# Performance work log

Hardware: AMD Instinct MI355X
Metric: run time of the kernel (lower is better)

The kernel has to match this reference:

```python
import jax, jax.numpy as jnp
import numpy as np

MU = 255          # mu-law levels - 1
H = 64            # block_hidden_size
SKIP = 256        # skip_size
NL = 24           # num_layers
CYC = 6           # cycle_size -> dilation = 2**(i % CYC)
UPK = 4           # upsample conv kernel/stride
REP = 75          # upsample repeat
LF = 80           # local_features_size
B = 2
LLEN = 64                      # local (spectrogram) frames
SLEN = LLEN * UPK * REP        # 19200 signal samples


def setup_inputs() -> dict:
    key = jax.random.key(0)
    ks = jax.random.split(key, 16)
    s = 0.1
    rn = lambda k, shape: jax.random.normal(k, shape, jnp.float32) * s
    return {
        "local_features": jax.random.normal(ks[0], (B, LLEN, LF), jnp.float32),
        "gold_signal": jax.random.randint(ks[1], (B, SLEN), 0, MU + 1, jnp.int32),
        "embed_W": rn(ks[2], (H, MU + 1)),          # 1x1 conv (mu+1 -> H), as matrix
        "embed_b": rn(ks[3], (H,)),
        "up_W": rn(ks[4], (LF, LF, UPK)),           # ConvTranspose1d weight [in, out, k]
        "up_b": rn(ks[5], (LF,)),
        "cond_W": rn(ks[6], (NL * 2 * H, LF)),      # 1x1 conv LF -> NL*2H
        "cond_b": rn(ks[7], (NL * 2 * H,)),
        "dil_W": rn(ks[8], (NL, 2 * H, H, 2)),      # dilated causal conv, kernel 2
        "dil_b": rn(ks[9], (NL, 2 * H)),
        "skip_W": rn(ks[10], (NL, SKIP, H)),
        "skip_b": rn(ks[11], (NL, SKIP)),
        "res_W": rn(ks[12], (NL - 1, H, H)),        # no residual conv on last layer
        "res_b": rn(ks[13], (NL - 1, H)),
        "out_W1": rn(ks[14], (MU + 1, SKIP)),       # out conv 1 (no bias)
        "out_W2": rn(ks[15], (MU + 1, MU + 1)),     # out conv 2 (no bias)
    }


def reference(local_features, gold_signal, embed_W, embed_b, up_W, up_b,
              cond_W, cond_b, dil_W, dil_b, skip_W, skip_b, res_W, res_b,
              out_W1, out_W2):
    Bv = local_features.shape[0]
    # --- conditional features upsample ---
    x = jnp.transpose(local_features, (0, 2, 1))                     # [B, LF, Lloc]
    # ConvTranspose1d with kernel == stride == UPK: each frame emits UPK frames
    up = jnp.einsum('bct,cok->botk', x, up_W).reshape(Bv, LF, -1)    # [B, LF, Lloc*UPK]
    up = up + up_b[None, :, None]
    up = jnp.repeat(up, REP, axis=-1)                                # [B, LF, SLEN]
    cond = jnp.einsum('oc,bct->bot', cond_W, up) + cond_b[None, :, None]
    L = cond.shape[-1]
    cond = cond.reshape(Bv, NL, 2 * H, L)                            # per-layer 2H channels
    # --- embed mu-law one-hot signal (one-hot matmul == gather) ---
    sig = jnp.transpose(embed_W[:, gold_signal], (1, 0, 2)) + embed_b[None, :, None]  # [B, H, L]
    # --- residual blocks ---
    skip_sum = jnp.zeros((Bv, SKIP, L), cond.dtype)
    for i in range(NL):
        d = 2 ** (i % CYC)
        prev = jnp.pad(sig, ((0, 0), (0, 0), (d, 0)))[:, :, :L]      # causal shift by dilation
        a = (jnp.einsum('oc,bct->bot', dil_W[i, :, :, 0], prev)
             + jnp.einsum('oc,bct->bot', dil_W[i, :, :, 1], sig)
             + dil_b[i][None, :, None] + cond[:, i])
        z = jnp.tanh(a[:, :H]) * jax.nn.sigmoid(a[:, H:])            # gated activation
        skip_sum = skip_sum + jnp.einsum('oc,bct->bot', skip_W[i], z) + skip_b[i][None, :, None]
        if i < NL - 1:
            sig = sig + jnp.einsum('oc,bct->bot', res_W[i], z) + res_b[i][None, :, None]
    # --- output head: ReLU -> 1x1 -> ReLU -> 1x1 -> log_softmax over levels ---
    h = jax.nn.relu(skip_sum)
    h = jax.nn.relu(jnp.einsum('oc,bct->bot', out_W1, h))
    logits = jnp.einsum('oc,bct->bot', out_W2, h)
    return jax.nn.log_softmax(logits, axis=1)                        # [B, mu+1, SLEN]
```

## Files before the change

kernel.cpp:

```cpp
#include <hip/hip_runtime.h>
#include <math.h>

#define MU1   256
#define H     64
#define H2    128
#define SKIPC 256
#define NL    24
#define LF    80
#define UPK   4
#define REP   75
#define BB    2
#define LLEN  64
#define LL    19200

using bf16x8 = __attribute__((ext_vector_type(8))) short;
using bf16x4 = __attribute__((ext_vector_type(4))) short;
using f32x4  = __attribute__((ext_vector_type(4))) float;

__device__ __forceinline__ float b2f(short s) {
    union { unsigned u; float f; } v; v.u = ((unsigned)(unsigned short)s) << 16; return v.f;
}
__device__ __forceinline__ short f2b(float f) {
    union { float f; unsigned u; } v; v.f = f;
    unsigned r = (v.u + 0x7fff + ((v.u >> 16) & 1)) >> 16;
    return (short)r;
}

__global__ __launch_bounds__(256) void prep_kernel(
    const float* __restrict__ dil_W,  const float* __restrict__ skip_W,
    const float* __restrict__ res_W,  const float* __restrict__ embed_W,
    const float* __restrict__ embed_b,const float* __restrict__ cond_W,
    const float* __restrict__ out_W1, const float* __restrict__ out_W2,
    const float* __restrict__ skip_b,
    short* __restrict__ dil_Wb, short* __restrict__ skip_Wb,
    short* __restrict__ res_Wb, short* __restrict__ embed_allb,
    float* __restrict__ cond_Wt, short* __restrict__ W1b,
    short* __restrict__ W2b, float* __restrict__ sbsum)
{
    int idx = blockIdx.x * 256 + threadIdx.x;
    const int n1 = NL * 2 * H2 * H;
    const int n2 = NL * SKIPC * H;
    const int n3 = (NL - 1) * H * H;
    const int n4 = MU1 * H;
    const int n5 = LF * NL * H2;
    const int n6 = MU1 * SKIPC;
    const int n7 = MU1 * MU1;
    if (idx < n1) {
        int c = idx & 63; int o = (idx >> 6) & 127;
        int k = (idx >> 13) & 1; int i = idx >> 14;
        dil_Wb[idx] = f2b(dil_W[((i * H2 + o) * H + c) * 2 + k]);
        return;
    }
    idx -= n1;
    if (idx < n2) { skip_Wb[idx] = f2b(skip_W[idx]); return; }
    idx -= n2;
    if (idx < n3) { res_Wb[idx] = f2b(res_W[idx]); return; }
    idx -= n3;
    if (idx < n4) {
        int h = idx & 63; int g = idx >> 6;
        embed_allb[idx] = f2b(embed_W[h * MU1 + g] + embed_b[h]);
        return;
    }
    idx -= n4;
    if (idx < n5) {
        int o = idx % (NL * H2); int c = idx / (NL * H2);
        cond_Wt[idx] = cond_W[o * LF + c];
        return;
    }
    idx -= n5;
    if (idx < n6) { W1b[idx] = f2b(out_W1[idx]); return; }
    idx -= n6;
    if (idx < n7) { W2b[idx] = f2b(out_W2[idx]); return; }
    idx -= n7;
    if (idx < SKIPC) {
        float a = 0.f;
        for (int i = 0; i < NL; i++) a += skip_b[i * SKIPC + idx];
        sbsum[idx] = a;
        return;
    }
}

__global__ __launch_bounds__(256) void embed_kernel(
    const int* __restrict__ gold, const short* __restrict__ eW,
    short* __restrict__ sig)
{
    int idx = blockIdx.x * 256 + threadIdx.x;
    if (idx >= BB * LL * 8) return;
    int ch = idx & 7; int bt = idx >> 3;
    int g = gold[bt];
    *(bf16x8*)(sig + (size_t)bt * H + ch * 8) = *(const bf16x8*)(eW + g * H + ch * 8);
}

__global__ __launch_bounds__(256) void cond_kernel(
    const float* __restrict__ lf, const float* __restrict__ up_W,
    const float* __restrict__ up_b, const float* __restrict__ cond_Wt,
    const float* __restrict__ cond_b, const float* __restrict__ dil_b,
    float* __restrict__ condS)
{
    __shared__ float s_up[LF];
    int j = blockIdx.x;
    int ot = blockIdx.y;
    int b = blockIdx.z;
    int frame = j >> 2, k = j & 3;
    int tid = threadIdx.x;
    if (tid < LF) {
        float a = up_b[tid];
        const float* lfr = lf + (b * LLEN + frame) * LF;
        #pragma unroll 8
        for (int c = 0; c < LF; ++c) a += lfr[c] * up_W[(c * LF + tid) * UPK + k];
        s_up[tid] = a;
    }
    __syncthreads();
    int o = ot * 256 + tid;
    float a = cond_b[o] + dil_b[o];
    #pragma unroll 8
    for (int c = 0; c < LF; ++c) a += cond_Wt[c * 3072 + o] * s_up[c];
    condS[((size_t)(b * 256 + j)) * 3072 + o] = a;
}

template<int DA, int DB, bool LASTPAIR>
__global__ __launch_bounds__(256) void pair_mfma(
    const short* __restrict__ sig_in, short* __restrict__ sig_out,
    short* __restrict__ z_grp,
    const short* __restrict__ dil_Wb_all,
    const short* __restrict__ res_Wb_all,
    const float* __restrict__ res_b_all,
    const float* __restrict__ condS,
    int p)
{
    __shared__ __align__(16) short sa[144][72];
    __shared__ __align__(16) short sb[128][72];
    __shared__ __align__(16) short sz[128][72];
    __shared__ float scond[2][3][128];

    const int iA = 2 * p, iB = 2 * p + 1;
    const int ilA = iA & 7, ilB = iB & 7;
    const int b = blockIdx.y;
    const int t0 = blockIdx.x * 96;
    const int tid = threadIdx.x;
    const int w = tid >> 6;
    const int lane = tid & 63;
    const int lr = lane & 15, lg = lane >> 4;
    const int c0 = (t0 >= 32) ? (t0 - 32) / 75 : 0;

    {
        const short* basein = sig_in + (size_t)b * LL * H;
        #pragma unroll
        for (int it = 0; it < 5; ++it) {
            int task = tid + it * 256;
            if (task < 1152) {
                int r = task >> 3, ch = task & 7;
                int t = t0 - 48 + r;
                bf16x8 v = {};
                if (t >= 0) v = *(const bf16x8*)(basein + (size_t)t * H + ch * 8);
                *(bf16x8*)&sa[r][ch * 8] = v;
            }
        }
        #pragma unroll
        for (int it = 0; it < 3; ++it) {
            int task = tid + it * 256;
            int sel = task >= 384;
            int cj = (task - sel * 384) >> 7;
            int o = task & 127;
            int col = c0 + cj; col = col > 255 ? 255 : col;
            scond[sel][cj][o] = condS[((size_t)(b * 256 + col)) * 3072 + (iA + sel) * 128 + o];
        }
    }
    __syncthreads();

    {
        const short* dW = dil_Wb_all + (size_t)iA * 2 * H2 * H;
        f32x4 acc[2][8];
        #pragma unroll
        for (int m = 0; m < 2; ++m)
            #pragma unroll
            for (int n = 0; n < 8; ++n) acc[m][n] = (f32x4){0.f, 0.f, 0.f, 0.f};
        bf16x8 afA[2][4];
        #pragma unroll
        for (int m = 0; m < 2; ++m) {
            int rc = 16 + 16 * (2 * w + m) + lr;
            afA[m][0] = *(const bf16x8*)&sa[rc - DA][lg * 8];
            afA[m][1] = *(const bf16x8*)&sa[rc - DA][32 + lg * 8];
            afA[m][2] = *(const bf16x8*)&sa[rc][lg * 8];
            afA[m][3] = *(const bf16x8*)&sa[rc][32 + lg * 8];
        }
        #pragma unroll
        for (int n = 0; n < 8; ++n)
            #pragma unroll
            for (int kk = 0; kk < 4; ++kk) {
                bf16x8 bw = *(const bf16x8*)(dW + (((kk >> 1) * H2 + 16 * n + lr) * H) + (kk & 1) * 32 + lg * 8);
                acc[0][n] = __builtin_amdgcn_mfma_f32_16x16x32_bf16(afA[0][kk], bw, acc[0][n], 0, 0, 0);
                acc[1][n] = __builtin_amdgcn_mfma_f32_16x16x32_bf16(afA[1][kk], bw, acc[1][n], 0, 0, 0);
            }
        #pragma unroll
        for (int m = 0; m < 2; ++m)
            #pragma unroll
            for (int n = 0; n < 4; ++n)
                #pragma unroll
                for (int r = 0; r < 4; ++r) {
                    int relt = -32 + 16 * (2 * w + m) + 4 * lg + r;
                    int t = t0 + relt;
                    int o = 16 * n + lr;
                    short zb = 0;
                    if (t >= 0) {
                        int ci = t / 75 - c0;
                        float av = acc[m][n][r] + scond[0][ci][o];
                        float gv = acc[m][n + 4][r] + scond[0][ci][64 + o];
                        float th = 1.f - 2.f / (__expf(2.f * av) + 1.f);
                        float sg = 1.f / (1.f + __expf(-gv));
                        zb = f2b(th * sg);
                    }
                    sz[relt + 32][o] = zb;
                }
    }
    __syncthreads();

    #pragma unroll
    for (int it = 0; it < 3; ++it) {
        int task = tid + it * 256;
        int r = task >> 3, ch = task & 7;
        *(bf16x8*)(z_grp + ((size_t)(b * LL + t0 + r)) * 512 + ilA * 64 + ch * 8)
            = *(const bf16x8*)&sz[32 + r][ch * 8];
    }

    {
        const short* rW = res_Wb_all + (size_t)iA * H * H;
        const float* rb_ = res_b_all + (size_t)iA * H;
        f32x4 rac[2][4];
        #pragma unroll
        for (int m = 0; m < 2; ++m)
            #pragma unroll
            for (int n = 0; n < 4; ++n) rac[m][n] = (f32x4){0.f, 0.f, 0.f, 0.f};
        bf16x8 za[2][2];
        #pragma unroll
        for (int m = 0; m < 2; ++m) {
            int row = 16 * (2 * w + m) + lr;
            za[m][0] = *(const bf16x8*)&sz[row][lg * 8];
            za[m][1] = *(const bf16x8*)&sz[row][32 + lg * 8];
        }
        #pragma unroll
        for (int n = 0; n < 4; ++n)
            #pragma unroll
            for (int kk = 0; kk < 2; ++kk) {
                bf16x8 bw = *(const bf16x8*)(rW + (16 * n + lr) * H + kk * 32 + lg * 8);
                rac[0][n] = __builtin_amdgcn_mfma_f32_16x16x32_bf16(za[0][kk], bw, rac[0][n], 0, 0, 0);
                rac[1][n] = __builtin_amdgcn_mfma_f32_16x16x32_bf16(za[1][kk], bw, rac[1][n], 0, 0, 0);
            }
        #pragma unroll
        for (int n = 0; n < 4; ++n) {
            float rbv = rb_[16 * n + lr];
            #pragma unroll
            for (int m = 0; m < 2; ++m)
                #pragma unroll
                for (int r = 0; r < 4; ++r) {
                    int relt = -32 + 16 * (2 * w + m) + 4 * lg + r;
                    int t = t0 + relt;
                    int c = 16 * n + lr;
                    short vb = 0;
                    if (t >= 0) vb = f2b(b2f(sa[relt + 48][c]) + rac[m][n][r] + rbv);
                    sb[relt + 32][c] = vb;
                }
        }
    }
    __syncthreads();

    {
        const short* dW = dil_Wb_all + (size_t)iB * 2 * H2 * H;
        f32x4 accF[6], accG[6];
        #pragma unroll
        for (int m = 0; m < 6; ++m) { accF[m] = (f32x4){0.f,0.f,0.f,0.f}; accG[m] = (f32x4){0.f,0.f,0.f,0.f}; }
        bf16x8 bwF[4], bwG[4];
        #pragma unroll
        for (int kk = 0; kk < 4; ++kk) {
            int oF = 16 * w + lr;
            bwF[kk] = *(const bf16x8*)(dW + (((kk >> 1) * H2 + oF) * H) + (kk & 1) * 32 + lg * 8);
            bwG[kk] = *(const bf16x8*)(dW + (((kk >> 1) * H2 + 64 + oF) * H) + (kk & 1) * 32 + lg * 8);
        }
        #pragma unroll
        for (int m = 0; m < 6; ++m) {
            int rc = 32 + 16 * m + lr;
            bf16x8 af[4];
            af[0] = *(const bf16x8*)&sb[rc - DB][lg * 8];
            af[1] = *(const bf16x8*)&sb[rc - DB][32 + lg * 8];
            af[2] = *(const bf16x8*)&sb[rc][lg * 8];
            af[3] = *(const bf16x8*)&sb[rc][32 + lg * 8];
            #pragma unroll
            for (int kk = 0; kk < 4; ++kk)
                accF[m] = __builtin_amdgcn_mfma_f32_16x16x32_bf16(af[kk], bwF[kk], accF[m], 0, 0, 0);
            #pragma unroll
            for (int kk = 0; kk < 4; ++kk)
                accG[m] = __builtin_amdgcn_mfma_f32_16x16x32_bf16(af[kk], bwG[kk], accG[m], 0, 0, 0);
        }
        #pragma unroll
        for (int m = 0; m < 6; ++m)
            #pragma unroll
            for (int r = 0; r < 4; ++r) {
                int relt = 16 * m + 4 * lg + r;
                int t = t0 + relt;
                int o = 16 * w + lr;
                int ci = t / 75 - c0;
                float av = accF[m][r] + scond[1][ci][o];
                float gv = accG[m][r] + scond[1][ci][64 + o];
                float th = 1.f - 2.f / (__expf(2.f * av) + 1.f);
                float sg = 1.f / (1.f + __expf(-gv));
                sz[relt][o] = f2b(th * sg);
            }
    }
    __syncthreads();

    #pragma unroll
    for (int it = 0; it < 3; ++it) {
        int task = tid + it * 256;
        int r = task >> 3, ch = task & 7;
        *(bf16x8*)(z_grp + ((size_t)(b * LL + t0 + r)) * 512 + ilB * 64 + ch * 8)
            = *(const bf16x8*)&sz[r][ch * 8];
    }

    if (!LASTPAIR) {
        const short* rW = res_Wb_all + (size_t)iB * H * H;
        const float* rb_ = res_b_all + (size_t)iB * H;
        int c = 16 * w + lr;
        f32x4 rac[6];
        #pragma unroll
        for (int m = 0; m < 6; ++m) rac[m] = (f32x4){0.f, 0.f, 0.f, 0.f};
        bf16x8 bwR[2];
        bwR[0] = *(const bf16x8*)(rW + c * H + lg * 8);
        bwR[1] = *(const bf16x8*)(rW + c * H + 32 + lg * 8);
        #pragma unroll
        for (int m = 0; m < 6; ++m) {
            bf16x8 z0 = *(const bf16x8*)&sz[16 * m + lr][lg * 8];
            bf16x8 z1 = *(const bf16x8*)&sz[16 * m + lr][32 + lg * 8];
            rac[m] = __builtin_amdgcn_mfma_f32_16x16x32_bf16(z0, bwR[0], rac[m], 0, 0, 0);
            rac[m] = __builtin_amdgcn_mfma_f32_16x16x32_bf16(z1, bwR[1], rac[m], 0, 0, 0);
        }
        float rbv = rb_[c];
        #pragma unroll
        for (int m = 0; m < 6; ++m)
            #pragma unroll
            for (int r = 0; r < 4; ++r) {
                int relt = 16 * m + 4 * lg + r;
                sa[relt][c] = f2b(b2f(sb[relt + 32][c]) + rac[m][r] + rbv);
            }
        __syncthreads();
        #pragma unroll
        for (int it = 0; it < 3; ++it) {
            int task = tid + it * 256;
            int r = task >> 3, ch = task & 7;
            *(bf16x8*)(sig_out + ((size_t)(b * LL + t0 + r)) * H + ch * 8)
                = *(const bf16x8*)&sa[r][ch * 8];
        }
    }
}

template<bool G0>
__global__ __launch_bounds__(256) void skip_gemm(
    const short* __restrict__ z_grp, const short* __restrict__ sWb,
    float* __restrict__ skipS)
{
    __shared__ __align__(16) short s_a[64][136];
    const int b = blockIdx.y;
    const int t0 = blockIdx.x * 64;
    const int tid = threadIdx.x;
    const int w = tid >> 6;
    const int lane = tid & 63;
    const int lr = lane & 15, lg = lane >> 4;

    f32x4 acc[4][4];
    #pragma unroll
    for (int mt = 0; mt < 4; ++mt)
        #pragma unroll
        for (int nt = 0; nt < 4; ++nt) acc[mt][nt] = (f32x4){0.f, 0.f, 0.f, 0.f};

    for (int chunk = 0; chunk < 4; ++chunk) {
        __syncthreads();
        #pragma unroll
        for (int it = 0; it < 4; ++it) {
            int task = tid + it * 256;
            int r = task >> 4, ch = task & 15;
            *(bf16x8*)&s_a[r][ch * 8] =
                *(const bf16x8*)(z_grp + ((size_t)(b * LL + t0 + r)) * 512 + chunk * 128 + ch * 8);
        }
        __syncthreads();
        bf16x8 bw[4][4];
        #pragma unroll
        for (int nt = 0; nt < 4; ++nt)
            #pragma unroll
            for (int kk = 0; kk < 4; ++kk) {
                int layer = 2 * chunk + (kk >> 1);
                bw[nt][kk] = *(const bf16x8*)(sWb +
                    ((size_t)(layer * SKIPC + 64 * w + 16 * nt + lr)) * H + (kk & 1) * 32 + 8 * lg);
            }
        #pragma unroll
        for (int mt = 0; mt < 4; ++mt) {
            bf16x8 afr[4];
            #pragma unroll
            for (int kk = 0; kk < 4; ++kk)
                afr[kk] = *(const bf16x8*)&s_a[16 * mt + lr][32 * kk + 8 * lg];
            #pragma unroll
            for (int nt = 0; nt < 4; ++nt)
                #pragma unroll
                for (int kk = 0; kk < 4; ++kk)
                    acc[mt][nt] = __builtin_amdgcn_mfma_f32_16x16x32_bf16(afr[kk], bw[nt][kk], acc[mt][nt], 0, 0, 0);
        }
    }
    #pragma unroll
    for (int mt = 0; mt < 4; ++mt)
        #pragma unroll
        for (int nt = 0; nt < 4; ++nt) {
            int s = 64 * w + 16 * nt + lr;
            #pragma unroll
            for (int reg = 0; reg < 4; ++reg) {
                int t = t0 + 16 * mt + 4 * lg + reg;
                float* p = skipS + ((size_t)(b * LL + t)) * SKIPC + s;
                float v = acc[mt][nt][reg];
                if (!G0) v += *p;
                *p = v;
            }
        }
}

__global__ __launch_bounds__(256) void head_mfma(
    const float* __restrict__ skipS, const float* __restrict__ sbsum,
    const short* __restrict__ W1b, const short* __restrict__ W2b,
    float* __restrict__ out)
{
    __shared__ __align__(16) unsigned char smem[128 * 68 * 4];
    short (*s_x)[264] = (short(*)[264])smem;
    float (*s_o)[68]  = (float(*)[68])smem;
    __shared__ float s_red[4][64];
    __shared__ float s_sb[256];

    const int b = blockIdx.y;
    const int t0 = blockIdx.x * 64;
    const int tid = threadIdx.x;
    const int w = tid >> 6;
    const int lane = tid & 63;
    const int lr = lane & 15, lg = lane >> 4;

    s_sb[tid] = sbsum[tid];
    __syncthreads();

    #pragma unroll
    for (int it = 0; it < 16; ++it) {
        int task = tid + it * 256;
        int r = task >> 6, c4 = task & 63;
        f32x4 v = *(const f32x4*)(skipS + ((size_t)(b * LL + t0 + r)) * SKIPC + c4 * 4);
        bf16x4 o;
        #pragma unroll
        for (int j = 0; j < 4; ++j) o[j] = f2b(fmaxf(v[j] + s_sb[c4 * 4 + j], 0.f));
        *(bf16x4*)&s_x[r][c4 * 4] = o;
    }
    __syncthreads();

    f32x4 acc1[4][4];
    #pragma unroll
    for (int mt = 0; mt < 4; ++mt)
        #pragma unroll
        for (int nt = 0; nt < 4; ++nt) acc1[mt][nt] = (f32x4){0.f, 0.f, 0.f, 0.f};
    #pragma unroll
    for (int kk = 0; kk < 8; ++kk) {
        bf16x8 afr[4];
        #pragma unroll
        for (int mt = 0; mt < 4; ++mt)
            afr[mt] = *(const bf16x8*)&s_x[16 * mt + lr][32 * kk + 8 * lg];
        #pragma unroll
        for (int nt = 0; nt < 4; ++nt) {
            bf16x8 bw = *(const bf16x8*)(W1b + ((size_t)(64 * w + 16 * nt + lr)) * MU1 + 32 * kk + 8 * lg);
            #pragma unroll
            for (int mt = 0; mt < 4; ++mt)
                acc1[mt][nt] = __builtin_amdgcn_mfma_f32_16x16x32_bf16(afr[mt], bw, acc1[mt][nt], 0, 0, 0);
        }
    }
    __syncthreads();
    #pragma unroll
    for (int mt = 0; mt < 4; ++mt)
        #pragma unroll
        for (int nt = 0; nt < 4; ++nt)
            #pragma unroll
            for (int reg = 0; reg < 4; ++reg) {
                int tl = 16 * mt + 4 * lg + reg;
                int o = 64 * w + 16 * nt + lr;
                s_x[tl][o] = f2b(fmaxf(acc1[mt][nt][reg], 0.f));
            }
    __syncthreads();

    f32x4 acc2[4][4];
    #pragma unroll
    for (int mt = 0; mt < 4; ++mt)
        #pragma unroll
        for (int nt = 0; nt < 4; ++nt) acc2[mt][nt] = (f32x4){0.f, 0.f, 0.f, 0.f};
    #pragma unroll
    for (int kk = 0; kk < 8; ++kk) {
        bf16x8 afr[4];
        #pragma unroll
        for (int mt = 0; mt < 4; ++mt)
            afr[mt] = *(const bf16x8*)&s_x[16 * mt + lr][32 * kk + 8 * lg];
        #pragma unroll
        for (int nt = 0; nt < 4; ++nt) {
            bf16x8 bw = *(const bf16x8*)(W2b + ((size_t)(64 * w + 16 * nt + lr)) * MU1 + 32 * kk + 8 * lg);
            #pragma unroll
            for (int mt = 0; mt < 4; ++mt)
                acc2[mt][nt] = __builtin_amdgcn_mfma_f32_16x16x32_bf16(afr[mt], bw, acc2[mt][nt], 0, 0, 0);
        }
    }

    float mv[4][4];
    #pragma unroll
    for (int mt = 0; mt < 4; ++mt)
        #pragma unroll
        for (int reg = 0; reg < 4; ++reg) {
            float m = -3.4e38f;
            #pragma unroll
            for (int nt = 0; nt < 4; ++nt) m = fmaxf(m, acc2[mt][nt][reg]);
            #pragma unroll
            for (int off = 1; off <= 8; off <<= 1) m = fmaxf(m, __shfl_xor(m, off));
            int tl = 16 * mt + 4 * lg + reg;
            if (lr == 0) s_red[w][tl] = m;
        }
    __syncthreads();
    #pragma unroll
    for (int mt = 0; mt < 4; ++mt)
        #pragma unroll
        for (int reg = 0; reg < 4; ++reg) {
            int tl = 16 * mt + 4 * lg + reg;
            mv[mt][reg] = fmaxf(fmaxf(s_red[0][tl], s_red[1][tl]), fmaxf(s_red[2][tl], s_red[3][tl]));
        }
    __syncthreads();
    #pragma unroll
    for (int mt = 0; mt < 4; ++mt)
        #pragma unroll
        for (int reg = 0; reg < 4; ++reg) {
            float s = 0.f;
            #pragma unroll
            for (int nt = 0; nt < 4; ++nt) s += __expf(acc2[mt][nt][reg] - mv[mt][reg]);
            #pragma unroll
            for (int off = 1; off <= 8; off <<= 1) s += __shfl_xor(s, off);
            int tl = 16 * mt + 4 * lg + reg;
            if (lr == 0) s_red[w][tl] = s;
        }
    __syncthreads();
    #pragma unroll
    for (int mt = 0; mt < 4; ++mt)
        #pragma unroll
        for (int reg = 0; reg < 4; ++reg) {
            int tl = 16 * mt + 4 * lg + reg;
            float denom = s_red[0][tl] + s_red[1][tl] + s_red[2][tl] + s_red[3][tl];
            mv[mt][reg] = mv[mt][reg] + __logf(denom);
        }
    __syncthreads();

    #pragma unroll
    for (int pass = 0; pass < 2; ++pass) {
        if ((w >> 1) == pass) {
            #pragma unroll
            for (int mt = 0; mt < 4; ++mt)
                #pragma unroll
                for (int nt = 0; nt < 4; ++nt)
                    #pragma unroll
                    for (int reg = 0; reg < 4; ++reg) {
                        int ch = 64 * (w & 1) + 16 * nt + lr;
                        int tl = 16 * mt + 4 * lg + reg;
                        s_o[ch][tl] = acc2[mt][nt][reg] - mv[mt][reg];
                    }
        }
        __syncthreads();
        {
            int row = tid >> 1, half = tid & 1;
            float* op = out + ((size_t)(b * MU1 + pass * 128 + row)) * LL + t0 + half * 32;
            #pragma unroll
            for (int k = 0; k < 8; ++k)
                *(f32x4*)(op + 4 * k) = *(const f32x4*)&s_o[row][half * 32 + 4 * k];
        }
        __syncthreads();
    }
}

extern "C" void kernel_launch(void* const* d_in, const int* in_sizes, int n_in,
                              void* d_out, int out_size, void* d_ws, size_t ws_size,
                              hipStream_t stream)
{
    const float* lf      = (const float*)d_in[0];
    const int*   gold    = (const int*)  d_in[1];
    const float* embed_W = (const float*)d_in[2];
    const float* embed_b = (const float*)d_in[3];
    const float* up_W    = (const float*)d_in[4];
    const float* up_b    = (const float*)d_in[5];
    const float* cond_W  = (const float*)d_in[6];
    const float* cond_b  = (const float*)d_in[7];
    const float* dil_W   = (const float*)d_in[8];
    const float* dil_b   = (const float*)d_in[9];
    const float* skip_W  = (const float*)d_in[10];
    const float* skip_b  = (const float*)d_in[11];
    const float* res_W   = (const float*)d_in[12];
    const float* res_b   = (const float*)d_in[13];
    const float* W1      = (const float*)d_in[14];
    const float* W2      = (const float*)d_in[15];
    float* out = (float*)d_out;

    unsigned char* p = (unsigned char*)d_ws;
    short* sigA      = (short*)p; p += (size_t)BB * LL * H * 2;
    short* sigB      = (short*)p; p += (size_t)BB * LL * H * 2;
    short* z_grp     = (short*)p; p += (size_t)BB * LL * 512 * 2;
    float* skipS     = (float*)p; p += (size_t)BB * LL * SKIPC * 4;
    float* condS     = (float*)p; p += (size_t)BB * 256 * NL * H2 * 4;
    short* dil_Wb    = (short*)p; p += (size_t)NL * 2 * H2 * H * 2;
    short* skip_Wb   = (short*)p; p += (size_t)NL * SKIPC * H * 2;
    short* res_Wb    = (short*)p; p += (size_t)(NL - 1) * H * H * 2;
    short* embed_allb= (short*)p; p += (size_t)MU1 * H * 2;
    float* cond_Wt   = (float*)p; p += (size_t)LF * NL * H2 * 4;
    short* W1b       = (short*)p; p += (size_t)MU1 * SKIPC * 2;
    short* W2b       = (short*)p; p += (size_t)MU1 * MU1 * 2;
    float* sbsum     = (float*)p; p += (size_t)SKIPC * 4;

    const int prep_n = NL*2*H2*H + NL*SKIPC*H + (NL-1)*H*H + MU1*H + LF*NL*H2 + MU1*SKIPC + MU1*MU1 + SKIPC;
    prep_kernel<<<(prep_n + 255) / 256, 256, 0, stream>>>(
        dil_W, skip_W, res_W, embed_W, embed_b, cond_W, W1, W2, skip_b,
        dil_Wb, skip_Wb, res_Wb, embed_allb, cond_Wt, W1b, W2b, sbsum);

    embed_kernel<<<(BB * LL * 8 + 255) / 256, 256, 0, stream>>>(gold, embed_allb, sigA);

    cond_kernel<<<dim3(256, 12, BB), 256, 0, stream>>>(lf, up_W, up_b, cond_Wt, cond_b, dil_b, condS);

    short* si = sigA;
    short* so = sigB;
    dim3 pgrid(LL / 96, BB);
    dim3 sgrid(LL / 64, BB);
    for (int pp = 0; pp < 12; ++pp) {
        int r3 = pp % 3;
        if (r3 == 0)
            pair_mfma<1, 2, false><<<pgrid, 256, 0, stream>>>(si, so, z_grp, dil_Wb, res_Wb, res_b, condS, pp);
        else if (r3 == 1)
            pair_mfma<4, 8, false><<<pgrid, 256, 0, stream>>>(si, so, z_grp, dil_Wb, res_Wb, res_b, condS, pp);
        else if (pp == 11)
            pair_mfma<16, 32, true><<<pgrid, 256, 0, stream>>>(si, so, z_grp, dil_Wb, res_Wb, res_b, condS, pp);
        else
            pair_mfma<16, 32, false><<<pgrid, 256, 0, stream>>>(si, so, z_grp, dil_Wb, res_Wb, res_b, condS, pp);
        short* tmp = si; si = so; so = tmp;

        if ((pp & 3) == 3) {
            int g = pp >> 2;
            const short* sWb = skip_Wb + (size_t)g * 8 * SKIPC * H;
            if (g == 0)
                skip_gemm<true><<<sgrid, 256, 0, stream>>>(z_grp, sWb, skipS);
            else
                skip_gemm<false><<<sgrid, 256, 0, stream>>>(z_grp, sWb, skipS);
        }
    }

    head_mfma<<<sgrid, 256, 0, stream>>>(skipS, sbsum, W1b, W2b, out);
}
```

Before: 591.1 us.

## Merge skip GEMM into following pair kernel via extra blocks and double-buffered z

Double-buffers the z group buffer so the skip GEMM for one group of 8 layers can run as extra blocks inside the next pair_mfma launch instead of as a separate launch. This removes two kernel launches and their serialisation, letting skip accumulation overlap with the residual-block work. It also halves the head kernel's time tile to 32 to launch more blocks. It needs extra workspace and falls back to the old schedule when the workspace is too small.

```diff
diff --git a/kernel.cpp b/kernel.cpp
--- a/kernel.cpp
+++ b/kernel.cpp
@@ -118,10 +118,84 @@
     condS[((size_t)(b * 256 + j)) * 3072 + o] = a;
 }
 
-template<int DA, int DB, bool LASTPAIR>
+template<bool G0>
+__device__ __forceinline__ void skip_body(
+    const short* __restrict__ z_grp, const short* __restrict__ sWb,
+    float* __restrict__ skipS, int b, int t0, int tid, short (*s_a)[136])
+{
+    const int w = tid >> 6;
+    const int lane = tid & 63;
+    const int lr = lane & 15, lg = lane >> 4;
+
+    f32x4 acc[4][4];
+    #pragma unroll
+    for (int mt = 0; mt < 4; ++mt)
+        #pragma unroll
+        for (int nt = 0; nt < 4; ++nt) acc[mt][nt] = (f32x4){0.f, 0.f, 0.f, 0.f};
+
+    for (int chunk = 0; chunk < 4; ++chunk) {
+        __syncthreads();
+        #pragma unroll
+        for (int it = 0; it < 4; ++it) {
+            int task = tid + it * 256;
+            int r = task >> 4, ch = task & 15;
+            *(bf16x8*)&s_a[r][ch * 8] =
+                *(const bf16x8*)(z_grp + ((size_t)(b * LL + t0 + r)) * 512 + chunk * 128 + ch * 8);
+        }
+        __syncthreads();
+        bf16x8 bw[4][4];
+        #pragma unroll
+        for (int nt = 0; nt < 4; ++nt)
+            #pragma unroll
+            for (int kk = 0; kk < 4; ++kk) {
+                int layer = 2 * chunk + (kk >> 1);
+                bw[nt][kk] = *(const bf16x8*)(sWb +
+                    ((size_t)(layer * SKIPC + 64 * w + 16 * nt + lr)) * H + (kk & 1) * 32 + 8 * lg);
+            }
+        #pragma unroll
+        for (int mt = 0; mt < 4; ++mt) {
+            bf16x8 afr[4];
+            #pragma unroll
+            for (int kk = 0; kk < 4; ++kk)
+                afr[kk] = *(const bf16x8*)&s_a[16 * mt + lr][32 * kk + 8 * lg];
+            #pragma unroll
+            for (int nt = 0; nt < 4; ++nt)
+                #pragma unroll
+                for (int kk = 0; kk < 4; ++kk)
+                    acc[mt][nt] = __builtin_amdgcn_mfma_f32_16x16x32_bf16(afr[kk], bw[nt][kk], acc[mt][nt], 0, 0, 0);
+        }
+    }
+    #pragma unroll
+    for (int mt = 0; mt < 4; ++mt)
+        #pragma unroll
+        for (int nt = 0; nt < 4; ++nt) {
+            int s = 64 * w + 16 * nt + lr;
+            #pragma unroll
+            for (int reg = 0; reg < 4; ++reg) {
+                int t = t0 + 16 * mt + 4 * lg + reg;
+                float* p = skipS + ((size_t)(b * LL + t)) * SKIPC + s;
+                float v = acc[mt][nt][reg];
+                if (!G0) v += *p;
+                *p = v;
+            }
+        }
+}
+
+template<bool G0>
+__global__ __launch_bounds__(256) void skip_gemm(
+    const short* __restrict__ z_grp, const short* __restrict__ sWb,
+    float* __restrict__ skipS)
+{
+    __shared__ __align__(16) short s_a[64][136];
+    skip_body<G0>(z_grp, sWb, skipS, blockIdx.y, blockIdx.x * 64, threadIdx.x, s_a);
+}
+
+template<int DA, int DB, bool LASTPAIR, bool MERGE, bool SG0>
 __global__ __launch_bounds__(256) void pair_mfma(
     const short* __restrict__ sig_in, short* __restrict__ sig_out,
-    short* __restrict__ z_grp,
+    short* __restrict__ z_wr,
+    const short* __restrict__ z_rd, const short* __restrict__ sWb,
+    float* __restrict__ skipS,
     const short* __restrict__ dil_Wb_all,
     const short* __restrict__ res_Wb_all,
     const float* __restrict__ res_b_all,
@@ -132,6 +206,13 @@
     __shared__ __align__(16) short sb[128][72];
     __shared__ __align__(16) short sz[128][72];
     __shared__ float scond[2][3][128];
+
+    if (MERGE && (int)blockIdx.x >= (LL / 96)) {
+        skip_body<SG0>(z_rd, sWb, skipS, blockIdx.y,
+                       ((int)blockIdx.x - LL / 96) * 64, threadIdx.x,
+                       (short(*)[136])&sa[0][0]);
+        return;
+    }
 
     const int iA = 2 * p, iB = 2 * p + 1;
     const int ilA = iA & 7, ilB = iB & 7;
@@ -219,7 +300,7 @@
     for (int it = 0; it < 3; ++it) {
         int task = tid + it * 256;
         int r = task >> 3, ch = task & 7;
-        *(bf16x8*)(z_grp + ((size_t)(b * LL + t0 + r)) * 512 + ilA * 64 + ch * 8)
+        *(bf16x8*)(z_wr + ((size_t)(b * LL + t0 + r)) * 512 + ilA * 64 + ch * 8)
             = *(const bf16x8*)&sz[32 + r][ch * 8];
     }
 
@@ -312,7 +393,7 @@
     for (int it = 0; it < 3; ++it) {
         int task = tid + it * 256;
         int r = task >> 3, ch = task & 7;
-        *(bf16x8*)(z_grp + ((size_t)(b * LL + t0 + r)) * 512 + ilB * 64 + ch * 8)
+        *(bf16x8*)(z_wr + ((size_t)(b * LL + t0 + r)) * 512 + ilB * 64 + ch * 8)
             = *(const bf16x8*)&sz[r][ch * 8];
     }
 
@@ -352,96 +433,29 @@
     }
 }
 
-template<bool G0>
-__global__ __launch_bounds__(256) void skip_gemm(
-    const short* __restrict__ z_grp, const short* __restrict__ sWb,
-    float* __restrict__ skipS)
-{
-    __shared__ __align__(16) short s_a[64][136];
+__global__ __launch_bounds__(256) void head_mfma(
+    const float* __restrict__ skipS, const float* __restrict__ sbsum,
+    const short* __restrict__ W1b, const short* __restrict__ W2b,
+    float* __restrict__ out)
+{
+    __shared__ __align__(16) unsigned char smem[18432];
+    short (*s_x)[264] = (short(*)[264])smem;
+    float (*s_o)[36]  = (float(*)[36])smem;
+    __shared__ float s_red[4][32];
+    __shared__ float s_sb[256];
+
     const int b = blockIdx.y;
-    const int t0 = blockIdx.x * 64;
+    const int t0 = blockIdx.x * 32;
     const int tid = threadIdx.x;
     const int w = tid >> 6;
     const int lane = tid & 63;
     const int lr = lane & 15, lg = lane >> 4;
 
-    f32x4 acc[4][4];
-    #pragma unroll
-    for (int mt = 0; mt < 4; ++mt)
-        #pragma unroll
-        for (int nt = 0; nt < 4; ++nt) acc[mt][nt] = (f32x4){0.f, 0.f, 0.f, 0.f};
-
-    for (int chunk = 0; chunk < 4; ++chunk) {
-        __syncthreads();
-        #pragma unroll
-        for (int it = 0; it < 4; ++it) {
-            int task = tid + it * 256;
-            int r = task >> 4, ch = task & 15;
-            *(bf16x8*)&s_a[r][ch * 8] =
-                *(const bf16x8*)(z_grp + ((size_t)(b * LL + t0 + r)) * 512 + chunk * 128 + ch * 8);
-        }
-        __syncthreads();
-        bf16x8 bw[4][4];
-        #pragma unroll
-        for (int nt = 0; nt < 4; ++nt)
-            #pragma unroll
-            for (int kk = 0; kk < 4; ++kk) {
-                int layer = 2 * chunk + (kk >> 1);
-                bw[nt][kk] = *(const bf16x8*)(sWb +
-                    ((size_t)(layer * SKIPC + 64 * w + 16 * nt + lr)) * H + (kk & 1) * 32 + 8 * lg);
-            }
-        #pragma unroll
-        for (int mt = 0; mt < 4; ++mt) {
-            bf16x8 afr[4];
-            #pragma unroll
-            for (int kk = 0; kk < 4; ++kk)
-                afr[kk] = *(const bf16x8*)&s_a[16 * mt + lr][32 * kk + 8 * lg];
-            #pragma unroll
-            for (int nt = 0; nt < 4; ++nt)
-                #pragma unroll
-                for (int kk = 0; kk < 4; ++kk)
-                    acc[mt][nt] = __builtin_amdgcn_mfma_f32_16x16x32_bf16(afr[kk], bw[nt][kk], acc[mt][nt], 0, 0, 0);
-        }
-    }
-    #pragma unroll
-    for (int mt = 0; mt < 4; ++mt)
-        #pragma unroll
-        for (int nt = 0; nt < 4; ++nt) {
-            int s = 64 * w + 16 * nt + lr;
-            #pragma unroll
-            for (int reg = 0; reg < 4; ++reg) {
-                int t = t0 + 16 * mt + 4 * lg + reg;
-                float* p = skipS + ((size_t)(b * LL + t)) * SKIPC + s;
-                float v = acc[mt][nt][reg];
-                if (!G0) v += *p;
-                *p = v;
-            }
-        }
-}
-
-__global__ __launch_bounds__(256) void head_mfma(
-    const float* __restrict__ skipS, const float* __restrict__ sbsum,
-    const short* __restrict__ W1b, const short* __restrict__ W2b,
-    float* __restrict__ out)
-{
-    __shared__ __align__(16) unsigned char smem[128 * 68 * 4];
-    short (*s_x)[264] = (short(*)[264])smem;
-    float (*s_o)[68]  = (float(*)[68])smem;
-    __shared__ float s_red[4][64];
-    __shared__ float s_sb[256];
-
-    const int b = blockIdx.y;
-    const int t0 = blockIdx.x * 64;
-    const int tid = threadIdx.x;
-    const int w = tid >> 6;
-    const int lane = tid & 63;
-    const int lr = lane & 15, lg = lane >> 4;
-
     s_sb[tid] = sbsum[tid];
     __syncthreads();
 
     #pragma unroll
-    for (int it = 0; it < 16; ++it) {
+    for (int it = 0; it < 8; ++it) {
         int task = tid + it * 256;
         int r = task >> 6, c4 = task & 63;
         f32x4 v = *(const f32x4*)(skipS + ((size_t)(b * LL + t0 + r)) * SKIPC + c4 * 4);
@@ -452,28 +466,28 @@
     }
     __syncthreads();
 
-    f32x4 acc1[4][4];
-    #pragma unroll
-    for (int mt = 0; mt < 4; ++mt)
+    f32x4 acc1[2][4];
+    #pragma unroll
+    for (int mt = 0; mt < 2; ++mt)
         #pragma unroll
         for (int nt = 0; nt < 4; ++nt) acc1[mt][nt] = (f32x4){0.f, 0.f, 0.f, 0.f};
     #pragma unroll
     for (int kk = 0; kk < 8; ++kk) {
-        bf16x8 afr[4];
-        #pragma unroll
-        for (int mt = 0; mt < 4; ++mt)
+        bf16x8 afr[2];
+        #pragma unroll
+        for (int mt = 0; mt < 2; ++mt)
             afr[mt] = *(const bf16x8*)&s_x[16 * mt + lr][32 * kk + 8 * lg];
         #pragma unroll
         for (int nt = 0; nt < 4; ++nt) {
             bf16x8 bw = *(const bf16x8*)(W1b + ((size_t)(64 * w + 16 * nt + lr)) * MU1 + 32 * kk + 8 * lg);
             #pragma unroll
-            for (int mt = 0; mt < 4; ++mt)
+            for (int mt = 0; mt < 2; ++mt)
                 acc1[mt][nt] = __builtin_amdgcn_mfma_f32_16x16x32_bf16(afr[mt], bw, acc1[mt][nt], 0, 0, 0);
         }
     }
     __syncthreads();
     #pragma unroll
-    for (int mt = 0; mt < 4; ++mt)
+    for (int mt = 0; mt < 2; ++mt)
         #pragma unroll
         for (int nt = 0; nt < 4; ++nt)
             #pragma unroll
@@ -484,29 +498,29 @@
             }
     __syncthreads();
 
-    f32x4 acc2[4][4];
-    #pragma unroll
-    for (int mt = 0; mt < 4; ++mt)
+    f32x4 acc2[2][4];
+    #pragma unroll
+    for (int mt = 0; mt < 2; ++mt)
         #pragma unroll
         for (int nt = 0; nt < 4; ++nt) acc2[mt][nt] = (f32x4){0.f, 0.f, 0.f, 0.f};
     #pragma unroll
     for (int kk = 0; kk < 8; ++kk) {
-        bf16x8 afr[4];
-        #pragma unroll
-        for (int mt = 0; mt < 4; ++mt)
+        bf16x8 afr[2];
+        #pragma unroll
+        for (int mt = 0; mt < 2; ++mt)
             afr[mt] = *(const bf16x8*)&s_x[16 * mt + lr][32 * kk + 8 * lg];
         #pragma unroll
         for (int nt = 0; nt < 4; ++nt) {
             bf16x8 bw = *(const bf16x8*)(W2b + ((size_t)(64 * w + 16 * nt + lr)) * MU1 + 32 * kk + 8 * lg);
             #pragma unroll
-            for (int mt = 0; mt < 4; ++mt)
+            for (int mt = 0; mt < 2; ++mt)
                 acc2[mt][nt] = __builtin_amdgcn_mfma_f32_16x16x32_bf16(afr[mt], bw, acc2[mt][nt], 0, 0, 0);
         }
     }
 
-    float mv[4][4];
-    #pragma unroll
-    for (int mt = 0; mt < 4; ++mt)
+    float mv[2][4];
+    #pragma unroll
+    for (int mt = 0; mt < 2; ++mt)
         #pragma unroll
         for (int reg = 0; reg < 4; ++reg) {
             float m = -3.4e38f;
@@ -519,7 +533,7 @@
         }
     __syncthreads();
     #pragma unroll
-    for (int mt = 0; mt < 4; ++mt)
+    for (int mt = 0; mt < 2; ++mt)
         #pragma unroll
         for (int reg = 0; reg < 4; ++reg) {
             int tl = 16 * mt + 4 * lg + reg;
@@ -527,7 +541,7 @@
         }
     __syncthreads();
     #pragma unroll
-    for (int mt = 0; mt < 4; ++mt)
+    for (int mt = 0; mt < 2; ++mt)
         #pragma unroll
         for (int reg = 0; reg < 4; ++reg) {
             float s = 0.f;
@@ -540,7 +554,7 @@
         }
     __syncthreads();
     #pragma unroll
-    for (int mt = 0; mt < 4; ++mt)
+    for (int mt = 0; mt < 2; ++mt)
         #pragma unroll
         for (int reg = 0; reg < 4; ++reg) {
             int tl = 16 * mt + 4 * lg + reg;
@@ -553,7 +567,7 @@
     for (int pass = 0; pass < 2; ++pass) {
         if ((w >> 1) == pass) {
             #pragma unroll
-            for (int mt = 0; mt < 4; ++mt)
+            for (int mt = 0; mt < 2; ++mt)
                 #pragma unroll
                 for (int nt = 0; nt < 4; ++nt)
                     #pragma unroll
@@ -566,10 +580,10 @@
         __syncthreads();
         {
             int row = tid >> 1, half = tid & 1;
-            float* op = out + ((size_t)(b * MU1 + pass * 128 + row)) * LL + t0 + half * 32;
-            #pragma unroll
-            for (int k = 0; k < 8; ++k)
-                *(f32x4*)(op + 4 * k) = *(const f32x4*)&s_o[row][half * 32 + 4 * k];
+            float* op = out + ((size_t)(b * MU1 + pass * 128 + row)) * LL + t0 + half * 16;
+            #pragma unroll
+            for (int k = 0; k < 4; ++k)
+                *(f32x4*)(op + 4 * k) = *(const f32x4*)&s_o[row][half * 16 + 4 * k];
         }
         __syncthreads();
     }
@@ -597,12 +611,24 @@
     const float* W2      = (const float*)d_in[15];
     float* out = (float*)d_out;
 
+    const size_t zbytes = (size_t)BB * LL * 512 * 2;
+    const size_t fixed  = (size_t)BB*LL*H*2*2
+                        + (size_t)BB*LL*SKIPC*4
+                        + (size_t)BB*256*NL*H2*4
+                        + (size_t)NL*2*H2*H*2 + (size_t)NL*SKIPC*H*2
+                        + (size_t)(NL-1)*H*H*2 + (size_t)MU1*H*2
+                        + (size_t)LF*NL*H2*4 + (size_t)MU1*SKIPC*2
+                        + (size_t)MU1*MU1*2 + (size_t)SKIPC*4 + 4096;
+    const bool overlap = ws_size >= fixed + 2 * zbytes;
+
     unsigned char* p = (unsigned char*)d_ws;
-    short* sigA      = (short*)p; p += (size_t)BB * LL * H * 2;
-    short* sigB      = (short*)p; p += (size_t)BB * LL * H * 2;
-    short* z_grp     = (short*)p; p += (size_t)BB * LL * 512 * 2;
-    float* skipS     = (float*)p; p += (size_t)BB * LL * SKIPC * 4;
-    float* condS     = (float*)p; p += (size_t)BB * 256 * NL * H2 * 4;
+    short* sigA  = (short*)p; p += (size_t)BB * LL * H * 2;
+    short* sigB  = (short*)p; p += (size_t)BB * LL * H * 2;
+    short* zbuf0 = (short*)p; p += zbytes;
+    short* zbuf1 = zbuf0;
+    if (overlap) { zbuf1 = (short*)p; p += zbytes; }
+    float* skipS = (float*)p; p += (size_t)BB * LL * SKIPC * 4;
+    float* condS = (float*)p; p += (size_t)BB * 256 * NL * H2 * 4;
     short* dil_Wb    = (short*)p; p += (size_t)NL * 2 * H2 * H * 2;
     short* skip_Wb   = (short*)p; p += (size_t)NL * SKIPC * H * 2;
     short* res_Wb    = (short*)p; p += (size_t)(NL - 1) * H * H * 2;
@@ -624,28 +650,43 @@
     short* si = sigA;
     short* so = sigB;
     dim3 pgrid(LL / 96, BB);
+    dim3 fgrid(LL / 96 + LL / 64, BB);
     dim3 sgrid(LL / 64, BB);
+
     for (int pp = 0; pp < 12; ++pp) {
+        short* zw = (overlap && pp >= 4 && pp < 8) ? zbuf1 : zbuf0;
         int r3 = pp % 3;
-        if (r3 == 0)
-            pair_mfma<1, 2, false><<<pgrid, 256, 0, stream>>>(si, so, z_grp, dil_Wb, res_Wb, res_b, condS, pp);
-        else if (r3 == 1)
-            pair_mfma<4, 8, false><<<pgrid, 256, 0, stream>>>(si, so, z_grp, dil_Wb, res_Wb, res_b, condS, pp);
-        else if (pp == 11)
-            pair_mfma<16, 32, true><<<pgrid, 256, 0, stream>>>(si, so, z_grp, dil_Wb, res_Wb, res_b, condS, pp);
-        else
-            pair_mfma<16, 32, false><<<pgrid, 256, 0, stream>>>(si, so, z_grp, dil_Wb, res_Wb, res_b, condS, pp);
+        if (overlap && pp == 4) {
+            pair_mfma<4, 8, false, true, true><<<fgrid, 256, 0, stream>>>(
+                si, so, zw, zbuf0, skip_Wb, skipS, dil_Wb, res_Wb, res_b, condS, pp);
+        } else if (overlap && pp == 8) {
+            pair_mfma<16, 32, false, true, false><<<fgrid, 256, 0, stream>>>(
+                si, so, zw, zbuf1, skip_Wb + (size_t)1 * 8 * SKIPC * H, skipS,
+                dil_Wb, res_Wb, res_b, condS, pp);
+        } else if (r3 == 0) {
+            pair_mfma<1, 2, false, false, false><<<pgrid, 256, 0, stream>>>(
+                si, so, zw, nullptr, nullptr, nullptr, dil_Wb, res_Wb, res_b, condS, pp);
+        } else if (r3 == 1) {
+            pair_mfma<4, 8, false, false, false><<<pgrid, 256, 0, stream>>>(
+                si, so, zw, nullptr, nullptr, nullptr, dil_Wb, res_Wb, res_b, condS, pp);
+        } else if (pp == 11) {
+            pair_mfma<16, 32, true, false, false><<<pgrid, 256, 0, stream>>>(
+                si, so, zw, nullptr, nullptr, nullptr, dil_Wb, res_Wb, res_b, condS, pp);
+        } else {
+            pair_mfma<16, 32, false, false, false><<<pgrid, 256, 0, stream>>>(
+                si, so, zw, nullptr, nullptr, nullptr, dil_Wb, res_Wb, res_b, condS, pp);
+        }
         short* tmp = si; si = so; so = tmp;
 
-        if ((pp & 3) == 3) {
+        if (!overlap && (pp == 3 || pp == 7)) {
             int g = pp >> 2;
             const short* sWb = skip_Wb + (size_t)g * 8 * SKIPC * H;
-            if (g == 0)
-                skip_gemm<true><<<sgrid, 256, 0, stream>>>(z_grp, sWb, skipS);
-            else
-                skip_gemm<false><<<sgrid, 256, 0, stream>>>(z_grp, sWb, skipS);
-        }
-    }
-
-    head_mfma<<<sgrid, 256, 0, stream>>>(skipS, sbsum, W1b, W2b, out);
-}
+            if (g == 0) skip_gemm<true><<<sgrid, 256, 0, stream>>>(zbuf0, sWb, skipS);
+            else        skip_gemm<false><<<sgrid, 256, 0, stream>>>(zbuf0, sWb, skipS);
+        }
+    }
+
+    skip_gemm<false><<<sgrid, 256, 0, stream>>>(zbuf0, skip_Wb + (size_t)2 * 8 * SKIPC * H, skipS);
+
+    head_mfma<<<dim3(LL / 32, BB), 256, 0, stream>>>(skipS, sbsum, W1b, W2b, out);
+}
```

After: 577.1 us. -2.4%, faster.
